# Kernel tuning notes

Measured on AMD Instinct MI355X. Metric: run time of the kernel, lower is better.

## Reference

```python
import jax, jax.numpy as jnp
import numpy as np

SEQ, D = 4096, 1024  # vector_size == dimension == 1024


def setup_inputs() -> dict:
    key = jax.random.key(0)
    ks = jax.random.split(key, 7)
    s = 1.0 / np.sqrt(D)
    return {
        "X": jax.random.normal(ks[0], (SEQ, D), dtype=jnp.float32),
        "Wq": jax.random.normal(ks[1], (D, D), dtype=jnp.float32) * s,
        "bq": jax.random.normal(ks[2], (D,), dtype=jnp.float32) * s,
        "Wk": jax.random.normal(ks[3], (D, D), dtype=jnp.float32) * s,
        "bk": jax.random.normal(ks[4], (D,), dtype=jnp.float32) * s,
        "Wv": jax.random.normal(ks[5], (D, D), dtype=jnp.float32) * s,
        "bv": jax.random.normal(ks[6], (D,), dtype=jnp.float32) * s,
    }


def reference(X, Wq, bq, Wk, bk, Wv, bv):
    # Batched QKV projections (nn.Linear: x @ W^T + b), replacing the per-vector loop.
    Q = X @ Wq.T + bq            # [S, D]
    K = X @ Wk.T + bk            # [S, D]
    V = X @ Wv.T + bv            # [S, D]
    scale = 1.0 / jnp.sqrt(jnp.asarray(D, dtype=X.dtype))
    scores = (Q @ K.T) * scale   # [S, S]
    attn = jax.nn.softmax(scores, axis=1)
    return attn @ V              # [S, D]
```

## Files before the change

kernel.cpp:

```cpp
#include <hip/hip_runtime.h>
#include <hip/hip_bf16.h>
#include <stdint.h>


typedef __bf16 bf16_t;
typedef __bf16 bf16x4 __attribute__((ext_vector_type(4)));
typedef __bf16 bf16x8 __attribute__((ext_vector_type(8)));
typedef float f32x4 __attribute__((ext_vector_type(4)));

#define AS1 __attribute__((address_space(1)))
#define AS3 __attribute__((address_space(3)))

__device__ __forceinline__ void async_ld16(const void* g, void* l) {
  __builtin_amdgcn_global_load_lds((AS1 void*)g, (AS3 void*)l, 16, 0, 0);
}

template <int MODE>
__global__ __launch_bounds__(512, 4) void gemm2(
    const bf16_t* __restrict__ A, const bf16_t* __restrict__ B, const int ld,
    const int Klen, bf16_t* __restrict__ o0, bf16_t* __restrict__ o1,
    bf16_t* __restrict__ o2, const float* __restrict__ b0,
    const float* __restrict__ b1, const float* __restrict__ b2,
    float* __restrict__ fout, float* __restrict__ rowsum) {
  __shared__ bf16_t smem[24576];
  bf16_t* As = smem;
  bf16_t* Bs = smem + 16384;

  const int t = threadIdx.x;
  const int lane = t & 63;
  const int wave = t >> 6;
  const int wm = wave >> 1;
  const int wn = wave & 1;
  const int q = lane >> 4;
  const int l16 = lane & 15;
  const int xf = l16 & 7;

  int m0, n0, k0 = 0, zz = 0;
  const int bid = blockIdx.x;
  if constexpr (MODE == 0) {
    const int x = bid & 7, sl = bid >> 3;
    m0 = ((x >> 1) * 4 + (sl & 3)) * 256;
    n0 = ((x & 1) * 12 + (sl >> 2)) * 128;
  } else if constexpr (MODE == 1) {
    const int x = bid & 7, sl = bid >> 3;
    m0 = ((x >> 2) * 8 + (sl >> 3)) * 256;
    n0 = ((x & 3) * 8 + (sl & 7)) * 128;
  } else {
    const int x = bid & 7, sl = bid >> 3;
    zz = x >> 1;
    m0 = ((x & 1) * 8 + (sl >> 3)) * 256;
    n0 = (sl & 7) * 128;
    k0 = zz * Klen;
  }

  const int srow = t >> 3;
  const int c8s = ((t & 7) ^ (srow & 7)) * 8;
  const bf16_t* Ab = A + (size_t)(m0 + srow) * ld + k0 + c8s;
  const bf16_t* Bb = B + (size_t)(n0 + srow) * ld + k0 + c8s;
  const int tl8 = t * 8;

  const int ar = wm * 64 + l16;
  const int br = wn * 64 + l16;

  f32x4 acc[4][4];
  const f32x4 zero4 = {0.f, 0.f, 0.f, 0.f};
#pragma unroll
  for (int i = 0; i < 4; ++i)
#pragma unroll
    for (int j = 0; j < 4; ++j) acc[i][j] = zero4;

  for (int kt = 0; kt < Klen; kt += 64) {
#pragma unroll
    for (int rr = 0; rr < 4; ++rr)
      async_ld16(Ab + kt + (size_t)(rr * 64) * ld, As + rr * 4096 + tl8);
#pragma unroll
    for (int rr = 0; rr < 2; ++rr)
      async_ld16(Bb + kt + (size_t)(rr * 64) * ld, Bs + rr * 4096 + tl8);
    __syncthreads();

#pragma unroll
    for (int s = 0; s < 2; ++s) {
      const int cs = ((s * 4 + q) ^ xf) * 8;
      bf16x8 fa[4], fb[4];
#pragma unroll
      for (int im = 0; im < 4; ++im)
        fa[im] = *(const bf16x8*)(As + (ar + im * 16) * 64 + cs);
#pragma unroll
      for (int j = 0; j < 4; ++j)
        fb[j] = *(const bf16x8*)(Bs + (br + j * 16) * 64 + cs);
#pragma unroll
      for (int im = 0; im < 4; ++im)
#pragma unroll
        for (int j = 0; j < 4; ++j)
          acc[im][j] = __builtin_amdgcn_mfma_f32_16x16x32_bf16(
              fa[im], fb[j], acc[im][j], 0, 0, 0);
    }
    __syncthreads();
  }

  const int mBase = m0 + wm * 64 + q * 4;

  if constexpr (MODE == 0) {
    const int sel = n0 >> 10;
    const int nl0 = (n0 & 1023) + wn * 64 + l16;
    if (sel < 2) {
      const float* bias = (sel == 0) ? b0 : b1;
      const float sc = (sel == 0) ? 0.03125f : 1.0f;
      bf16_t* dst = (sel == 0) ? o0 : o1;
      float bb[4];
#pragma unroll
      for (int j = 0; j < 4; ++j) bb[j] = bias[nl0 + j * 16];
#pragma unroll
      for (int im = 0; im < 4; ++im) {
        const int mr = mBase + im * 16;
#pragma unroll
        for (int r = 0; r < 4; ++r)
#pragma unroll
          for (int j = 0; j < 4; ++j)
            dst[(size_t)(mr + r) * 1024 + nl0 + j * 16] =
                (bf16_t)((acc[im][j][r] + bb[j]) * sc);
      }
    } else {
      bf16_t* vs = smem;
      const int dg0 = n0 & 1023;
#pragma unroll
      for (int h = 0; h < 2; ++h) {
        if (wn == h) {
#pragma unroll
          for (int j = 0; j < 4; ++j) {
            const int dl = j * 16 + l16;
            const float bb = b2[dg0 + h * 64 + dl];
#pragma unroll
            for (int im = 0; im < 4; ++im) {
              bf16x4 v;
#pragma unroll
              for (int r = 0; r < 4; ++r) v[r] = (bf16_t)(acc[im][j][r] + bb);
              *(bf16x4*)(vs + dl * 264 + wm * 64 + im * 16 + q * 4) = v;
            }
          }
        }
        __syncthreads();
#pragma unroll
        for (int rr = 0; rr < 4; ++rr) {
          const int task = rr * 512 + t;
          const int row = task >> 5, ck = task & 31;
          *(bf16x8*)(o2 + (size_t)(dg0 + h * 64 + row) * 4096 + m0 + ck * 8) =
              *(const bf16x8*)(vs + row * 264 + ck * 8);
        }
        __syncthreads();
      }
    }
  } else if constexpr (MODE == 1) {
    float ps[4][4];
#pragma unroll
    for (int im = 0; im < 4; ++im)
#pragma unroll
      for (int r = 0; r < 4; ++r) ps[im][r] = 0.f;
    const int nb = n0 + wn * 64 + l16;
#pragma unroll
    for (int im = 0; im < 4; ++im) {
      const int mr = mBase + im * 16;
#pragma unroll
      for (int r = 0; r < 4; ++r)
#pragma unroll
        for (int j = 0; j < 4; ++j) {
          const float e = __expf(acc[im][j][r]);
          ps[im][r] += e;
          o0[(size_t)(mr + r) * 4096 + nb + j * 16] = (bf16_t)e;
        }
    }
#pragma unroll
    for (int im = 0; im < 4; ++im)
#pragma unroll
      for (int r = 0; r < 4; ++r) {
        float v = ps[im][r];
        v += __shfl_xor(v, 1);
        v += __shfl_xor(v, 2);
        v += __shfl_xor(v, 4);
        v += __shfl_xor(v, 8);
        ps[im][r] = v;
      }
    if (l16 == 0) {
#pragma unroll
      for (int im = 0; im < 4; ++im)
#pragma unroll
        for (int r = 0; r < 4; ++r)
          atomicAdd(rowsum + mBase + im * 16 + r, ps[im][r]);
    }
  } else {
    float inv[4][4];
#pragma unroll
    for (int im = 0; im < 4; ++im)
#pragma unroll
      for (int r = 0; r < 4; ++r)
        inv[im][r] = 1.0f / rowsum[mBase + im * 16 + r];
    const int nb = n0 + wn * 64 + l16;
    if (zz < 3) {
      bf16_t* pp = (zz == 0) ? o0 : ((zz == 1) ? o1 : o2);
#pragma unroll
      for (int im = 0; im < 4; ++im) {
        const int mr = mBase + im * 16;
#pragma unroll
        for (int r = 0; r < 4; ++r) {
          const float iv = inv[im][r];
#pragma unroll
          for (int j = 0; j < 4; ++j)
            pp[(size_t)(mr + r) * 1024 + nb + j * 16] =
                (bf16_t)(acc[im][j][r] * iv);
        }
      }
    } else {
#pragma unroll
      for (int im = 0; im < 4; ++im) {
        const int mr = mBase + im * 16;
#pragma unroll
        for (int r = 0; r < 4; ++r) {
          const float iv = inv[im][r];
#pragma unroll
          for (int j = 0; j < 4; ++j)
            fout[(size_t)(mr + r) * 1024 + nb + j * 16] = acc[im][j][r] * iv;
        }
      }
    }
  }
}

__global__ __launch_bounds__(256) void cvt_all(
    const float* __restrict__ X, const float* __restrict__ Wq,
    const float* __restrict__ Wk, const float* __restrict__ Wv,
    bf16_t* __restrict__ Xb, bf16_t* __restrict__ Wb,
    float* __restrict__ rowsum) {
  int i = blockIdx.x * 256 + threadIdx.x;
  if (i >= 1835008) {
    rowsum[i - 1835008] = 0.f;
    return;
  }
  const float* src;
  bf16_t* dst;
  int off;
  if (i < 1048576) {
    src = X; dst = Xb; off = i;
  } else {
    const int w = i - 1048576;
    const int sel = w >> 18;
    off = w & 0x3FFFF;
    src = (sel == 0) ? Wq : ((sel == 1) ? Wk : Wv);
    dst = Wb + (size_t)sel * (1024 * 1024);
  }
  const float4 v = ((const float4*)src)[off];
  bf16x4 o;
  o[0] = (bf16_t)v.x; o[1] = (bf16_t)v.y; o[2] = (bf16_t)v.z; o[3] = (bf16_t)v.w;
  ((bf16x4*)dst)[off] = o;
}

__global__ __launch_bounds__(256) void reduce_out(
    const bf16_t* __restrict__ p0, const bf16_t* __restrict__ p1,
    const bf16_t* __restrict__ p2, float* __restrict__ out) {
  const int i = blockIdx.x * 256 + threadIdx.x;
  const bf16x8 a = ((const bf16x8*)p0)[i];
  const bf16x8 b = ((const bf16x8*)p1)[i];
  const bf16x8 c = ((const bf16x8*)p2)[i];
  float4 lo = ((const float4*)out)[2 * i];
  float4 hi = ((const float4*)out)[2 * i + 1];
  lo.x += (float)a[0] + (float)b[0] + (float)c[0];
  lo.y += (float)a[1] + (float)b[1] + (float)c[1];
  lo.z += (float)a[2] + (float)b[2] + (float)c[2];
  lo.w += (float)a[3] + (float)b[3] + (float)c[3];
  hi.x += (float)a[4] + (float)b[4] + (float)c[4];
  hi.y += (float)a[5] + (float)b[5] + (float)c[5];
  hi.z += (float)a[6] + (float)b[6] + (float)c[6];
  hi.w += (float)a[7] + (float)b[7] + (float)c[7];
  ((float4*)out)[2 * i] = lo;
  ((float4*)out)[2 * i + 1] = hi;
}

extern "C" void kernel_launch(void* const* d_in, const int* in_sizes, int n_in,
                              void* d_out, int out_size, void* d_ws,
                              size_t ws_size, hipStream_t stream) {
  const int S = 4096, D = 1024;
  const float* X  = (const float*)d_in[0];
  const float* Wq = (const float*)d_in[1];
  const float* bq = (const float*)d_in[2];
  const float* Wk = (const float*)d_in[3];
  const float* bk = (const float*)d_in[4];
  const float* Wv = (const float*)d_in[5];
  const float* bv = (const float*)d_in[6];
  float* out = (float*)d_out;

  bf16_t* Xb = (bf16_t*)d_ws;
  bf16_t* Wb = Xb + (size_t)S * D;
  bf16_t* Qb = Wb + (size_t)3 * D * D;
  bf16_t* Kb = Qb + (size_t)S * D;
  bf16_t* Vt = Kb + (size_t)S * D;
  bf16_t* Sc = Vt + (size_t)D * S;
  float* rowsum = (float*)(Sc + (size_t)S * S);

  cvt_all<<<7184, 256, 0, stream>>>(X, Wq, Wk, Wv, Xb, Wb, rowsum);

  gemm2<0><<<384, 512, 0, stream>>>(
      Xb, Wb, D, D, Qb, Kb, Vt, bq, bk, bv, nullptr, nullptr);
  gemm2<1><<<512, 512, 0, stream>>>(
      Qb, Kb, D, D, Sc, nullptr, nullptr, nullptr, nullptr, nullptr, nullptr,
      rowsum);
  gemm2<2><<<512, 512, 0, stream>>>(
      Sc, Vt, S, S / 4, Xb, Qb, Kb, nullptr, nullptr, nullptr, out, rowsum);
  reduce_out<<<S * D / 8 / 256, 256, 0, stream>>>(Xb, Qb, Kb, out);
}
```

Baseline: 204.8 us.

## Load A fragments directly from global and double-buffer B tiles in LDS

The GEMM kernel is restructured so each wave owns a 32-row strip of A and reads its A fragments straight from global memory into registers, while only the B tile is staged in LDS with a double buffer. This lets the next B tile load overlap the current MFMA work and removes one barrier per iteration. The LDS footprint shrinks, and each wave now computes a 32x128 tile (2x8 MFMA blocks) instead of 64x64. The cost is that A is no longer shared through LDS, so global reads of A rise and are uncoalesced 16-byte per-lane loads whose latency sits directly in the compute loop.

```diff
diff --git a/kernel.cpp b/kernel.cpp
--- a/kernel.cpp
+++ b/kernel.cpp
@@ -16,21 +16,19 @@
 }
 
 template <int MODE>
-__global__ __launch_bounds__(512, 4) void gemm2(
+__global__ __launch_bounds__(512, 4) void gemm3(
     const bf16_t* __restrict__ A, const bf16_t* __restrict__ B, const int ld,
     const int Klen, bf16_t* __restrict__ o0, bf16_t* __restrict__ o1,
     bf16_t* __restrict__ o2, const float* __restrict__ b0,
     const float* __restrict__ b1, const float* __restrict__ b2,
     float* __restrict__ fout, float* __restrict__ rowsum) {
-  __shared__ bf16_t smem[24576];
-  bf16_t* As = smem;
-  bf16_t* Bs = smem + 16384;
+  __shared__ bf16_t smem[16896];
+  bf16_t* bufB0 = smem;
+  bf16_t* bufB1 = smem + 8192;
 
   const int t = threadIdx.x;
   const int lane = t & 63;
-  const int wave = t >> 6;
-  const int wm = wave >> 1;
-  const int wn = wave & 1;
+  const int w = t >> 6;
   const int q = lane >> 4;
   const int l16 = lane & 15;
   const int xf = l16 & 7;
@@ -55,68 +53,75 @@
 
   const int srow = t >> 3;
   const int c8s = ((t & 7) ^ (srow & 7)) * 8;
-  const bf16_t* Ab = A + (size_t)(m0 + srow) * ld + k0 + c8s;
   const bf16_t* Bb = B + (size_t)(n0 + srow) * ld + k0 + c8s;
   const int tl8 = t * 8;
 
-  const int ar = wm * 64 + l16;
-  const int br = wn * 64 + l16;
-
-  f32x4 acc[4][4];
+  const bf16_t* Ap = A + (size_t)(m0 + w * 32 + l16) * ld + k0 + q * 8;
+  const size_t a16 = (size_t)16 * ld;
+
+  f32x4 acc[2][8];
   const f32x4 zero4 = {0.f, 0.f, 0.f, 0.f};
 #pragma unroll
-  for (int i = 0; i < 4; ++i)
-#pragma unroll
-    for (int j = 0; j < 4; ++j) acc[i][j] = zero4;
-
-  for (int kt = 0; kt < Klen; kt += 64) {
-#pragma unroll
-    for (int rr = 0; rr < 4; ++rr)
-      async_ld16(Ab + kt + (size_t)(rr * 64) * ld, As + rr * 4096 + tl8);
-#pragma unroll
-    for (int rr = 0; rr < 2; ++rr)
-      async_ld16(Bb + kt + (size_t)(rr * 64) * ld, Bs + rr * 4096 + tl8);
-    __syncthreads();
+  for (int i = 0; i < 2; ++i)
+#pragma unroll
+    for (int j = 0; j < 8; ++j) acc[i][j] = zero4;
+
+  const int NT = Klen >> 6;
+
+  auto STAGE_B = [&](int T, bf16_t* buf) {
+    const int kk = T << 6;
+    async_ld16(Bb + kk, buf + tl8);
+    async_ld16(Bb + (size_t)64 * ld + kk, buf + 4096 + tl8);
+  };
+
+  STAGE_B(0, bufB0);
+  __syncthreads();
+
+  for (int T = 0; T < NT; ++T) {
+    bf16_t* cur = (T & 1) ? bufB1 : bufB0;
+    bf16_t* nxt = (T & 1) ? bufB0 : bufB1;
+    if (T + 1 < NT) STAGE_B(T + 1, nxt);
+    const int kk = T << 6;
 
 #pragma unroll
     for (int s = 0; s < 2; ++s) {
+      bf16x8 fa[2], fb[8];
+#pragma unroll
+      for (int im = 0; im < 2; ++im)
+        fa[im] = *(const bf16x8*)(Ap + (size_t)im * a16 + kk + s * 32);
       const int cs = ((s * 4 + q) ^ xf) * 8;
-      bf16x8 fa[4], fb[4];
-#pragma unroll
-      for (int im = 0; im < 4; ++im)
-        fa[im] = *(const bf16x8*)(As + (ar + im * 16) * 64 + cs);
-#pragma unroll
-      for (int j = 0; j < 4; ++j)
-        fb[j] = *(const bf16x8*)(Bs + (br + j * 16) * 64 + cs);
-#pragma unroll
-      for (int im = 0; im < 4; ++im)
-#pragma unroll
-        for (int j = 0; j < 4; ++j)
+#pragma unroll
+      for (int j = 0; j < 8; ++j)
+        fb[j] = *(const bf16x8*)(cur + (j * 16 + l16) * 64 + cs);
+#pragma unroll
+      for (int im = 0; im < 2; ++im)
+#pragma unroll
+        for (int j = 0; j < 8; ++j)
           acc[im][j] = __builtin_amdgcn_mfma_f32_16x16x32_bf16(
               fa[im], fb[j], acc[im][j], 0, 0, 0);
     }
     __syncthreads();
   }
 
-  const int mBase = m0 + wm * 64 + q * 4;
+  const int mBase = m0 + w * 32 + q * 4;
 
   if constexpr (MODE == 0) {
     const int sel = n0 >> 10;
-    const int nl0 = (n0 & 1023) + wn * 64 + l16;
+    const int nl0 = (n0 & 1023) + l16;
     if (sel < 2) {
       const float* bias = (sel == 0) ? b0 : b1;
       const float sc = (sel == 0) ? 0.03125f : 1.0f;
       bf16_t* dst = (sel == 0) ? o0 : o1;
-      float bb[4];
-#pragma unroll
-      for (int j = 0; j < 4; ++j) bb[j] = bias[nl0 + j * 16];
-#pragma unroll
-      for (int im = 0; im < 4; ++im) {
+      float bb[8];
+#pragma unroll
+      for (int j = 0; j < 8; ++j) bb[j] = bias[nl0 + j * 16];
+#pragma unroll
+      for (int im = 0; im < 2; ++im) {
         const int mr = mBase + im * 16;
 #pragma unroll
         for (int r = 0; r < 4; ++r)
 #pragma unroll
-          for (int j = 0; j < 4; ++j)
+          for (int j = 0; j < 8; ++j)
             dst[(size_t)(mr + r) * 1024 + nl0 + j * 16] =
                 (bf16_t)((acc[im][j][r] + bb[j]) * sc);
       }
@@ -125,18 +130,17 @@
       const int dg0 = n0 & 1023;
 #pragma unroll
       for (int h = 0; h < 2; ++h) {
-        if (wn == h) {
-#pragma unroll
-          for (int j = 0; j < 4; ++j) {
-            const int dl = j * 16 + l16;
-            const float bb = b2[dg0 + h * 64 + dl];
-#pragma unroll
-            for (int im = 0; im < 4; ++im) {
-              bf16x4 v;
-#pragma unroll
-              for (int r = 0; r < 4; ++r) v[r] = (bf16_t)(acc[im][j][r] + bb);
-              *(bf16x4*)(vs + dl * 264 + wm * 64 + im * 16 + q * 4) = v;
-            }
+#pragma unroll
+        for (int jj = 0; jj < 4; ++jj) {
+          const int dl = jj * 16 + l16;
+          const float bb = b2[dg0 + h * 64 + dl];
+#pragma unroll
+          for (int im = 0; im < 2; ++im) {
+            bf16x4 v;
+#pragma unroll
+            for (int r = 0; r < 4; ++r)
+              v[r] = (bf16_t)(acc[im][h * 4 + jj][r] + bb);
+            *(bf16x4*)(vs + dl * 264 + w * 32 + im * 16 + q * 4) = v;
           }
         }
         __syncthreads();
@@ -151,26 +155,26 @@
       }
     }
   } else if constexpr (MODE == 1) {
-    float ps[4][4];
-#pragma unroll
-    for (int im = 0; im < 4; ++im)
+    float ps[2][4];
+#pragma unroll
+    for (int im = 0; im < 2; ++im)
 #pragma unroll
       for (int r = 0; r < 4; ++r) ps[im][r] = 0.f;
-    const int nb = n0 + wn * 64 + l16;
-#pragma unroll
-    for (int im = 0; im < 4; ++im) {
+    const int nb = n0 + l16;
+#pragma unroll
+    for (int im = 0; im < 2; ++im) {
       const int mr = mBase + im * 16;
 #pragma unroll
       for (int r = 0; r < 4; ++r)
 #pragma unroll
-        for (int j = 0; j < 4; ++j) {
+        for (int j = 0; j < 8; ++j) {
           const float e = __expf(acc[im][j][r]);
           ps[im][r] += e;
           o0[(size_t)(mr + r) * 4096 + nb + j * 16] = (bf16_t)e;
         }
     }
 #pragma unroll
-    for (int im = 0; im < 4; ++im)
+    for (int im = 0; im < 2; ++im)
 #pragma unroll
       for (int r = 0; r < 4; ++r) {
         float v = ps[im][r];
@@ -182,42 +186,42 @@
       }
     if (l16 == 0) {
 #pragma unroll
-      for (int im = 0; im < 4; ++im)
+      for (int im = 0; im < 2; ++im)
 #pragma unroll
         for (int r = 0; r < 4; ++r)
           atomicAdd(rowsum + mBase + im * 16 + r, ps[im][r]);
     }
   } else {
-    float inv[4][4];
-#pragma unroll
-    for (int im = 0; im < 4; ++im)
+    float inv[2][4];
+#pragma unroll
+    for (int im = 0; im < 2; ++im)
 #pragma unroll
       for (int r = 0; r < 4; ++r)
         inv[im][r] = 1.0f / rowsum[mBase + im * 16 + r];
-    const int nb = n0 + wn * 64 + l16;
+    const int nb = n0 + l16;
     if (zz < 3) {
       bf16_t* pp = (zz == 0) ? o0 : ((zz == 1) ? o1 : o2);
 #pragma unroll
-      for (int im = 0; im < 4; ++im) {
+      for (int im = 0; im < 2; ++im) {
         const int mr = mBase + im * 16;
 #pragma unroll
         for (int r = 0; r < 4; ++r) {
           const float iv = inv[im][r];
 #pragma unroll
-          for (int j = 0; j < 4; ++j)
+          for (int j = 0; j < 8; ++j)
             pp[(size_t)(mr + r) * 1024 + nb + j * 16] =
                 (bf16_t)(acc[im][j][r] * iv);
         }
       }
     } else {
 #pragma unroll
-      for (int im = 0; im < 4; ++im) {
+      for (int im = 0; im < 2; ++im) {
         const int mr = mBase + im * 16;
 #pragma unroll
         for (int r = 0; r < 4; ++r) {
           const float iv = inv[im][r];
 #pragma unroll
-          for (int j = 0; j < 4; ++j)
+          for (int j = 0; j < 8; ++j)
             fout[(size_t)(mr + r) * 1024 + nb + j * 16] = acc[im][j][r] * iv;
         }
       }
@@ -297,12 +301,12 @@
 
   cvt_all<<<7184, 256, 0, stream>>>(X, Wq, Wk, Wv, Xb, Wb, rowsum);
 
-  gemm2<0><<<384, 512, 0, stream>>>(
+  gemm3<0><<<384, 512, 0, stream>>>(
       Xb, Wb, D, D, Qb, Kb, Vt, bq, bk, bv, nullptr, nullptr);
-  gemm2<1><<<512, 512, 0, stream>>>(
+  gemm3<1><<<512, 512, 0, stream>>>(
       Qb, Kb, D, D, Sc, nullptr, nullptr, nullptr, nullptr, nullptr, nullptr,
       rowsum);
-  gemm2<2><<<512, 512, 0, stream>>>(
+  gemm3<2><<<512, 512, 0, stream>>>(
       Sc, Vt, S, S / 4, Xb, Qb, Kb, nullptr, nullptr, nullptr, out, rowsum);
   reduce_out<<<S * D / 8 / 256, 256, 0, stream>>>(Xb, Qb, Kb, out);
 }
```

After: 222.3 us. +8.6%, slower.
